# Optimization experiments

Hardware: AMD Instinct MI355X
Metric: run time of the kernel (lower is better)

## Reference

```python
import jax, jax.numpy as jnp
import numpy as np

N_NODES = 100000
N_EDGES = 1600000
IN_C, HID_C, OUT_C = 128, 128, 64


def setup_inputs() -> dict:
    key = jax.random.key(0)
    k1, k2, k3, k4 = jax.random.split(key, 4)
    x = jax.random.normal(k1, (N_NODES, IN_C), dtype=jnp.float32)
    edge_index = jax.random.randint(k2, (2, N_EDGES), 0, N_NODES, dtype=jnp.int32)
    # Glorot-style init scale for the linear weights (matches PyG GCNConv default)
    W1 = jax.random.normal(k3, (IN_C, HID_C), dtype=jnp.float32) * (1.0 / np.sqrt(IN_C))
    b1 = jnp.zeros((HID_C,), dtype=jnp.float32)
    W2 = jax.random.normal(k4, (HID_C, OUT_C), dtype=jnp.float32) * (1.0 / np.sqrt(HID_C))
    b2 = jnp.zeros((OUT_C,), dtype=jnp.float32)
    return {"x": x, "edge_index": edge_index, "W1": W1, "b1": b1, "W2": W2, "b2": b2}


def _gcn_norm(edge_index, num_nodes):
    """Add self-loops and compute symmetric normalization deg^-1/2[src]*deg^-1/2[dst]."""
    src, dst = edge_index[0], edge_index[1]
    loop = jnp.arange(num_nodes, dtype=src.dtype)
    src_f = jnp.concatenate([src, loop])
    dst_f = jnp.concatenate([dst, loop])
    ones = jnp.ones_like(dst_f, dtype=jnp.float32)
    deg = jax.ops.segment_sum(ones, dst_f, num_segments=num_nodes)  # in-degree incl. self-loop
    deg_inv_sqrt = jnp.where(deg > 0, jax.lax.rsqrt(deg), 0.0)
    norm = deg_inv_sqrt[src_f] * deg_inv_sqrt[dst_f]  # [E+N]
    return src_f, dst_f, norm


def _gcn_conv(x, W, b, src_f, dst_f, norm, num_nodes):
    h = x @ W                              # [N, C_out] linear transform first
    msg = h[src_f] * norm[:, None]         # gather + scale, [E+N, C_out]
    agg = jax.ops.segment_sum(msg, dst_f, num_segments=num_nodes)  # scatter-add
    return agg + b


def reference(x, edge_index, W1, b1, W2, b2):
    n = x.shape[0]
    src_f, dst_f, norm = _gcn_norm(edge_index, n)
    h = jax.nn.relu(_gcn_conv(x, W1, b1, src_f, dst_f, norm, n))
    out = _gcn_conv(h, W2, b2, src_f, dst_f, norm, n)
    return out
```

## Files before the change

kernel.cpp:

```cpp
#include <hip/hip_runtime.h>


constexpr int BLK = 256;
constexpr int PCAP = 2560;
constexpr int CHUNK = 2048;
constexpr int NBMAX = 800;


__global__ __launch_bounds__(256)
void count_kernel(const int* __restrict__ dst, unsigned short* __restrict__ cnt,
                  int e, int nbuck) {
    __shared__ int hist[NBMAX];
    const int t = threadIdx.x;
    const int base = blockIdx.x * CHUNK;
    const int cend = min(CHUNK, e - base);

    for (int i = t; i < nbuck; i += 256) hist[i] = 0;
    __syncthreads();
    for (int i = t; i < cend; i += 256) atomicAdd(&hist[dst[base + i] >> 7], 1);
    __syncthreads();
    unsigned short* o = cnt + (size_t)blockIdx.x * nbuck;
    for (int i = t; i < nbuck; i += 256) o[i] = (unsigned short)hist[i];
}


__global__ __launch_bounds__(256)
void scan_bins_kernel(unsigned short* __restrict__ cnt, int* __restrict__ totals,
                      int nbuck, int nblk) {
    __shared__ int wsum[256];
    const int j = blockIdx.x;
    const int t = threadIdx.x;
    const int b0 = t * 4;
    int v[4];
    int s = 0;
#pragma unroll
    for (int q = 0; q < 4; ++q) {
        const int B = b0 + q;
        v[q] = (B < nblk) ? (int)cnt[(size_t)B * nbuck + j] : 0;
        s += v[q];
    }
    wsum[t] = s;
    __syncthreads();
    for (int off = 1; off < 256; off <<= 1) {
        int u = (t >= off) ? wsum[t - off] : 0;
        __syncthreads();
        wsum[t] += u;
        __syncthreads();
    }
    int run = (t > 0) ? wsum[t - 1] : 0;
#pragma unroll
    for (int q = 0; q < 4; ++q) {
        const int B = b0 + q;
        if (B < nblk) {
            cnt[(size_t)B * nbuck + j] = (unsigned short)min(run, PCAP);
            run += v[q];
        }
    }
    if (t == 255) totals[j] = run;
}


__global__ __launch_bounds__(256)
void place_kernel(const int* __restrict__ src, const int* __restrict__ dst,
                  const unsigned short* __restrict__ cnt, unsigned* __restrict__ ebuf,
                  int e, int nbuck) {
    __shared__ unsigned stage[CHUNK];
    __shared__ unsigned short keys[CHUNK];
    __shared__ int hist[NBMAX];
    __shared__ int excl[NBMAX];
    __shared__ int gbase[NBMAX];
    __shared__ int wsum[256];

    const int t = threadIdx.x;
    const int base = blockIdx.x * CHUNK;
    const int cend = min(CHUNK, e - base);

    for (int i = t; i < nbuck; i += 256) hist[i] = 0;
    __syncthreads();

    int dreg[8];
#pragma unroll
    for (int q = 0; q < 8; ++q) {
        const int i = t + q * 256;
        dreg[q] = (i < cend) ? dst[base + i] : -1;
        if (i < cend) atomicAdd(&hist[dreg[q] >> 7], 1);
    }
    __syncthreads();

    const int b0 = t * 4;
    int s0 = 0, s1 = 0, s2 = 0, s3 = 0;
    if (b0 < nbuck)     s0 = hist[b0];
    if (b0 + 1 < nbuck) s1 = hist[b0 + 1];
    if (b0 + 2 < nbuck) s2 = hist[b0 + 2];
    if (b0 + 3 < nbuck) s3 = hist[b0 + 3];
    wsum[t] = s0 + s1 + s2 + s3;
    __syncthreads();
    for (int off = 1; off < 256; off <<= 1) {
        int u = (t >= off) ? wsum[t - off] : 0;
        __syncthreads();
        wsum[t] += u;
        __syncthreads();
    }
    int run = (t > 0) ? wsum[t - 1] : 0;
    if (b0 < nbuck)     { excl[b0]     = run; hist[b0]     = run; run += s0; }
    if (b0 + 1 < nbuck) { excl[b0 + 1] = run; hist[b0 + 1] = run; run += s1; }
    if (b0 + 2 < nbuck) { excl[b0 + 2] = run; hist[b0 + 2] = run; run += s2; }
    if (b0 + 3 < nbuck) { excl[b0 + 3] = run; hist[b0 + 3] = run; run += s3; }
    {
        const unsigned short* cb = cnt + (size_t)blockIdx.x * nbuck;
        for (int i = t; i < nbuck; i += 256) gbase[i] = (int)cb[i];
    }
    __syncthreads();

#pragma unroll
    for (int q = 0; q < 8; ++q) {
        const int i = t + q * 256;
        if (i < cend) {
            const int s = src[base + i], d = dreg[q];
            const int bb = d >> 7;
            const int p = atomicAdd(&hist[bb], 1);
            stage[p] = ((unsigned)s << 7) | (unsigned)(d & 127);
            keys[p] = (unsigned short)bb;
        }
    }
    __syncthreads();

    for (int i = t; i < cend; i += 256) {
        const int bb = keys[i];
        const int p = gbase[bb] + (i - excl[bb]);
        if (p < PCAP) ebuf[(size_t)bb * PCAP + p] = stage[i];
    }
}


__global__ __launch_bounds__(256)
void build_kernel(const unsigned* __restrict__ ebuf, const int* __restrict__ totals,
                  float* __restrict__ dis, int2* __restrict__ rp,
                  int* __restrict__ esrc, int n) {
    __shared__ int packed[PCAP];
    __shared__ int sorted[PCAP];
    __shared__ unsigned short rank[PCAP];
    __shared__ int hist[128];
    __shared__ int excl[128];
    __shared__ int start[128];

    const int b = blockIdx.x, t = threadIdx.x;
    const int base = b << 7;
    const int nloc = min(128, n - base);
    const int tot = min(totals[b], PCAP);

    if (t < 128) hist[t] = 0;
    __syncthreads();

    const unsigned* eb = ebuf + (size_t)b * PCAP;
    for (int i = t; i < tot; i += 256) {
        int v = (int)eb[i];
        packed[i] = v;
        rank[i] = (unsigned short)atomicAdd(&hist[v & 127], 1);
    }
    __syncthreads();

    if (t < 128) excl[t] = hist[t];
    __syncthreads();
    for (int off = 1; off < 128; off <<= 1) {
        int v = (t >= off && t < 128) ? excl[t - off] : 0;
        __syncthreads();
        if (t < 128) excl[t] += v;
        __syncthreads();
    }

    if (t < 128) {
        int deg = hist[t];
        int st = excl[t] - deg;
        start[t] = st;
        if (t < nloc) {
            dis[base + t] = rsqrtf((float)(deg + 1));
            int gs = b * PCAP + st;
            rp[base + t] = make_int2(gs, gs + deg);
        }
    }
    __syncthreads();

    for (int i = t; i < tot; i += 256) {
        int v = packed[i];
        sorted[start[v & 127] + rank[i]] = v >> 7;
    }
    __syncthreads();

    if (t < 128) {
        const int s0 = start[t];
        const int e0 = s0 + hist[t];
        for (int i = s0 + 1; i < e0; ++i) {
            int v = sorted[i];
            int j = i - 1;
            while (j >= s0 && sorted[j] > v) { sorted[j + 1] = sorted[j]; --j; }
            sorted[j + 1] = v;
        }
    }
    __syncthreads();

    int* eo = esrc + b * PCAP;
    for (int i = t; i < tot; i += 256) eo[i] = sorted[i];
}


__device__ __forceinline__ unsigned short f2bf(float f) {
    unsigned u = __float_as_uint(f);
    u += 0x7fffu + ((u >> 16) & 1u);
    return (unsigned short)(u >> 16);
}
__device__ __forceinline__ float bflo(unsigned u) { return __uint_as_float(u << 16); }
__device__ __forceinline__ float bfhi(unsigned u) { return __uint_as_float(u & 0xffff0000u); }
__device__ __forceinline__ unsigned pk2(short a, short b) {
    return (unsigned)(unsigned short)a | ((unsigned)(unsigned short)b << 16);
}

__device__ __forceinline__ void split2(float v, short& hi, short& lo) {
    unsigned short h = f2bf(v);
    float hf = __uint_as_float(((unsigned)h) << 16);
    hi = (short)h;
    lo = (short)f2bf(v - hf);
}

typedef __attribute__((ext_vector_type(8))) short bf16x8;
typedef __attribute__((ext_vector_type(4))) float f32x4;
#define MFMA_B16(a, b, c) __builtin_amdgcn_mfma_f32_16x16x32_bf16(a, b, c, 0, 0, 0)

__device__ __forceinline__ void split8(const float4& a, const float4& b, bf16x8& h, bf16x8& l) {
    short hh, ll;
    split2(a.x, hh, ll); h[0] = hh; l[0] = ll;
    split2(a.y, hh, ll); h[1] = hh; l[1] = ll;
    split2(a.z, hh, ll); h[2] = hh; l[2] = ll;
    split2(a.w, hh, ll); h[3] = hh; l[3] = ll;
    split2(b.x, hh, ll); h[4] = hh; l[4] = ll;
    split2(b.y, hh, ll); h[5] = hh; l[5] = ll;
    split2(b.z, hh, ll); h[6] = hh; l[6] = ll;
    split2(b.w, hh, ll); h[7] = hh; l[7] = ll;
}


__global__ void prep_b_kernel(const float* __restrict__ W1, const float* __restrict__ W2,
                              unsigned short* __restrict__ B1h, unsigned short* __restrict__ B1l,
                              unsigned short* __restrict__ B2h, unsigned short* __restrict__ B2l) {
    const int c = blockIdx.x;
    const int k = threadIdx.x;
    short h, l;
    if (c < 128) {
        split2(W1[(size_t)k * 128 + c], h, l);
        B1h[c * 128 + k] = (unsigned short)h;
        B1l[c * 128 + k] = (unsigned short)l;
    } else {
        const int c2 = c - 128;
        split2(W2[(size_t)k * 64 + c2], h, l);
        B2h[c2 * 128 + k] = (unsigned short)h;
        B2l[c2 * 128 + k] = (unsigned short)l;
    }
}


constexpr int BAS = 72;

__global__ __launch_bounds__(256, 4)
void gemm_mfma(const float* __restrict__ Af,
               const unsigned short* __restrict__ Bh, const unsigned short* __restrict__ Bl,
               const float* __restrict__ dis, unsigned* __restrict__ Cb, int nrows) {
    constexpr int COLS = 128;
    constexpr int CT = COLS / 16;
    constexpr int BE = COLS * BAS;
    constexpr int CSC = COLS + 8;
    constexpr int SMEM = (2 * BE * 2 > 128 * CSC * 2) ? 2 * BE * 2 : 128 * CSC * 2;

    __shared__ __align__(16) char smem[SMEM];
    short* sBh = (short*)smem;
    short* sBl = sBh + BE;

    const int t = threadIdx.x;
    const int rowbase = blockIdx.x * 128;
    const int wave = t >> 6;
    const int lane = t & 63;
    const int quad = lane >> 4;
    const int l16 = lane & 15;

    const int gr0 = rowbase + wave * 32 + l16;
    const int gr1 = gr0 + 16;

    f32x4 acc[2][CT];
#pragma unroll
    for (int rt = 0; rt < 2; ++rt)
#pragma unroll
        for (int ct = 0; ct < CT; ++ct) {
            f32x4 z = {0.f, 0.f, 0.f, 0.f};
            acc[rt][ct] = z;
        }

    for (int half = 0; half < 2; ++half) {
        {
            constexpr int NV = COLS * 8;
            uint4* dh = (uint4*)sBh;
            uint4* dl = (uint4*)sBl;
            const uint4* gh = (const uint4*)Bh;
            const uint4* gl = (const uint4*)Bl;
            for (int idx = t; idx < NV; idx += 256) {
                int c = idx >> 3, kq = idx & 7;
                int gidx = c * 16 + half * 8 + kq;
                int didx = c * 9 + kq;
                dh[didx] = gh[gidx];
                dl[didx] = gl[gidx];
            }
        }
        __syncthreads();

#pragma unroll
        for (int kc = 0; kc < 2; ++kc) {
            const int ko = kc * 32 + quad * 8;
            bf16x8 ah0, al0, ah1, al1;
            float4 va = {0.f, 0.f, 0.f, 0.f}, vb = va, vc = va, vd = va;
            if (gr0 < nrows) {
                const float4* ap = (const float4*)(Af + (size_t)gr0 * 128 + half * 64 + ko);
                va = ap[0]; vb = ap[1];
            }
            if (gr1 < nrows) {
                const float4* ap = (const float4*)(Af + (size_t)gr1 * 128 + half * 64 + ko);
                vc = ap[0]; vd = ap[1];
            }
            split8(va, vb, ah0, al0);
            split8(vc, vd, ah1, al1);
#pragma unroll
            for (int ct = 0; ct < CT; ++ct) {
                const int bo = (ct * 16 + l16) * BAS + ko;
                bf16x8 bh = *(const bf16x8*)&sBh[bo];
                bf16x8 bl = *(const bf16x8*)&sBl[bo];
                acc[0][ct] = MFMA_B16(ah0, bh, acc[0][ct]);
                acc[1][ct] = MFMA_B16(ah1, bh, acc[1][ct]);
                acc[0][ct] = MFMA_B16(al0, bh, acc[0][ct]);
                acc[1][ct] = MFMA_B16(al1, bh, acc[1][ct]);
                acc[0][ct] = MFMA_B16(ah0, bl, acc[0][ct]);
                acc[1][ct] = MFMA_B16(ah1, bl, acc[1][ct]);
            }
        }
        __syncthreads();
    }

    short* Cs = (short*)smem;
    float sv[2][4];
#pragma unroll
    for (int rt = 0; rt < 2; ++rt)
#pragma unroll
        for (int r = 0; r < 4; ++r) {
            int rr = rowbase + wave * 32 + rt * 16 + quad * 4 + r;
            sv[rt][r] = (rr < nrows) ? dis[rr] : 0.f;
        }
#pragma unroll
    for (int rt = 0; rt < 2; ++rt)
#pragma unroll
        for (int ct = 0; ct < CT; ++ct) {
            const int rb = wave * 32 + rt * 16 + quad * 4;
            const int c = ct * 16 + l16;
#pragma unroll
            for (int r = 0; r < 4; ++r)
                Cs[(rb + r) * CSC + c] = (short)f2bf(sv[rt][r] * acc[rt][ct][r]);
        }
    __syncthreads();

    {
        const int row = t >> 1, hf = t & 1;
        const int gr = rowbase + row;
        if (gr < nrows) {
            const uint4* cr = (const uint4*)&Cs[row * CSC + hf * (COLS / 2)];
            uint4* dstp = (uint4*)Cb + (size_t)gr * (COLS / 8) + hf * (COLS / 16);
#pragma unroll
            for (int i = 0; i < COLS / 16; ++i) dstp[i] = cr[i];
        }
    }
}


#define ACC8(v)                                           \
    acc[0] += bflo(v.x); acc[1] += bfhi(v.x);             \
    acc[2] += bflo(v.y); acc[3] += bfhi(v.y);             \
    acc[4] += bflo(v.z); acc[5] += bfhi(v.z);             \
    acc[6] += bflo(v.w); acc[7] += bfhi(v.w);

__global__ __launch_bounds__(512)
void gather_gemm_kernel(const int2* __restrict__ rp, const int* __restrict__ esrc,
                        const float* __restrict__ dis, const unsigned* __restrict__ hs,
                        const float* __restrict__ bias,
                        const unsigned short* __restrict__ B2h,
                        const unsigned short* __restrict__ B2l,
                        unsigned* __restrict__ h2b, int n) {
    constexpr int ASTR = 136;
    constexpr int CSTR = 72;
    __shared__ __align__(16) short sAh[32 * ASTR];
    __shared__ __align__(16) short sAl[32 * ASTR];

    const int t = threadIdx.x;
    const int base = blockIdx.x * 32;

    {
        const int nl = t >> 4;
        const int lc = t & 15;
        const int node = base + nl;

        if (node < n) {
            const uint4* h4 = (const uint4*)hs;
            const int2 se = rp[node];
            float acc[8];
            {
                uint4 v = h4[(size_t)node * 16 + lc];
                acc[0] = bflo(v.x); acc[1] = bfhi(v.x);
                acc[2] = bflo(v.y); acc[3] = bfhi(v.y);
                acc[4] = bflo(v.z); acc[5] = bfhi(v.z);
                acc[6] = bflo(v.w); acc[7] = bfhi(v.w);
            }
            int k = se.x;
            const int end = se.y;
            for (; k + 3 < end; k += 4) {
                int s0 = esrc[k], s1 = esrc[k + 1], s2 = esrc[k + 2], s3 = esrc[k + 3];
                uint4 v0 = h4[(size_t)s0 * 16 + lc];
                uint4 v1 = h4[(size_t)s1 * 16 + lc];
                uint4 v2 = h4[(size_t)s2 * 16 + lc];
                uint4 v3 = h4[(size_t)s3 * 16 + lc];
                ACC8(v0) ACC8(v1) ACC8(v2) ACC8(v3)
            }
            for (; k < end; ++k) {
                uint4 v = h4[(size_t)esrc[k] * 16 + lc];
                ACC8(v)
            }

            const float di = dis[node];
            const float4 ba = ((const float4*)bias)[lc * 2];
            const float4 bb = ((const float4*)bias)[lc * 2 + 1];
            float v0 = fmaxf(fmaf(di, acc[0], ba.x), 0.f);
            float v1 = fmaxf(fmaf(di, acc[1], ba.y), 0.f);
            float v2 = fmaxf(fmaf(di, acc[2], ba.z), 0.f);
            float v3 = fmaxf(fmaf(di, acc[3], ba.w), 0.f);
            float v4 = fmaxf(fmaf(di, acc[4], bb.x), 0.f);
            float v5 = fmaxf(fmaf(di, acc[5], bb.y), 0.f);
            float v6 = fmaxf(fmaf(di, acc[6], bb.z), 0.f);
            float v7 = fmaxf(fmaf(di, acc[7], bb.w), 0.f);

            short h0, l0, h1, l1, h2, l2, h3, l3, h4v, l4, h5, l5, h6, l6, h7, l7;
            split2(v0, h0, l0); split2(v1, h1, l1); split2(v2, h2, l2); split2(v3, h3, l3);
            split2(v4, h4v, l4); split2(v5, h5, l5); split2(v6, h6, l6); split2(v7, h7, l7);
            uint4 oh, ol;
            oh.x = pk2(h0, h1); oh.y = pk2(h2, h3); oh.z = pk2(h4v, h5); oh.w = pk2(h6, h7);
            ol.x = pk2(l0, l1); ol.y = pk2(l2, l3); ol.z = pk2(l4, l5);  ol.w = pk2(l6, l7);
            *(uint4*)&sAh[nl * ASTR + lc * 8] = oh;
            *(uint4*)&sAl[nl * ASTR + lc * 8] = ol;
        } else {
            uint4 z = {0u, 0u, 0u, 0u};
            *(uint4*)&sAh[nl * ASTR + lc * 8] = z;
            *(uint4*)&sAl[nl * ASTR + lc * 8] = z;
        }
    }
    __syncthreads();

    const int wave = t >> 6, lane = t & 63, quad = lane >> 4, l16 = lane & 15;
    const int col = wave * 16 + l16;
    f32x4 c0 = {0.f, 0.f, 0.f, 0.f}, c1 = c0;
    if (t < 256) {
#pragma unroll
        for (int ks = 0; ks < 4; ++ks) {
            const int ko = ks * 32 + quad * 8;
            bf16x8 bh = *(const bf16x8*)&B2h[col * 128 + ko];
            bf16x8 bl = *(const bf16x8*)&B2l[col * 128 + ko];
            bf16x8 ah0 = *(const bf16x8*)&sAh[l16 * ASTR + ko];
            bf16x8 al0 = *(const bf16x8*)&sAl[l16 * ASTR + ko];
            bf16x8 ah1 = *(const bf16x8*)&sAh[(16 + l16) * ASTR + ko];
            bf16x8 al1 = *(const bf16x8*)&sAl[(16 + l16) * ASTR + ko];
            c0 = MFMA_B16(ah0, bh, c0);
            c1 = MFMA_B16(ah1, bh, c1);
            c0 = MFMA_B16(al0, bh, c0);
            c1 = MFMA_B16(al1, bh, c1);
            c0 = MFMA_B16(ah0, bl, c0);
            c1 = MFMA_B16(ah1, bl, c1);
        }
    }
    __syncthreads();

    short* Cs = sAh;
    if (t < 256) {
#pragma unroll
        for (int r = 0; r < 4; ++r) {
            const int row0 = quad * 4 + r, row1 = 16 + quad * 4 + r;
            const float d0 = (base + row0 < n) ? dis[base + row0] : 0.f;
            const float d1 = (base + row1 < n) ? dis[base + row1] : 0.f;
            Cs[row0 * CSTR + col] = (short)f2bf(d0 * c0[r]);
            Cs[row1 * CSTR + col] = (short)f2bf(d1 * c1[r]);
        }
    }
    __syncthreads();
    if (t < 256) {
        const int row = t >> 3, l8 = t & 7;
        const int gr = base + row;
        if (gr < n)
            ((uint4*)h2b)[(size_t)gr * 8 + l8] = *(const uint4*)&Cs[row * CSTR + l8 * 8];
    }
}


#define ACCLO(v)                                          \
    acc[0] += bflo(v.x); acc[1] += bfhi(v.x);             \
    acc[2] += bflo(v.y); acc[3] += bfhi(v.y);             \
    acc[4] += bflo(v.z); acc[5] += bfhi(v.z);             \
    acc[6] += bflo(v.w); acc[7] += bfhi(v.w);
#define ACCHI(v)                                          \
    acc[8]  += bflo(v.x); acc[9]  += bfhi(v.x);           \
    acc[10] += bflo(v.y); acc[11] += bfhi(v.y);           \
    acc[12] += bflo(v.z); acc[13] += bfhi(v.z);           \
    acc[14] += bflo(v.w); acc[15] += bfhi(v.w);

__global__ __launch_bounds__(256)
void gather_out_kernel(const int2* __restrict__ rp, const int* __restrict__ esrc,
                       const float* __restrict__ dis, const unsigned* __restrict__ hs,
                       const float* __restrict__ bias, float* __restrict__ out, int n) {
    const int gid = blockIdx.x * BLK + threadIdx.x;
    const int node = gid >> 2;
    const int l4 = gid & 3;
    if (node >= n) return;

    const uint4* h4 = (const uint4*)hs;
    const int2 se = rp[node];

    float acc[16];
    {
        uint4 v0 = h4[(size_t)node * 8 + l4];
        uint4 v1 = h4[(size_t)node * 8 + 4 + l4];
        acc[0] = bflo(v0.x); acc[1] = bfhi(v0.x);
        acc[2] = bflo(v0.y); acc[3] = bfhi(v0.y);
        acc[4] = bflo(v0.z); acc[5] = bfhi(v0.z);
        acc[6] = bflo(v0.w); acc[7] = bfhi(v0.w);
        acc[8]  = bflo(v1.x); acc[9]  = bfhi(v1.x);
        acc[10] = bflo(v1.y); acc[11] = bfhi(v1.y);
        acc[12] = bflo(v1.z); acc[13] = bfhi(v1.z);
        acc[14] = bflo(v1.w); acc[15] = bfhi(v1.w);
    }

    int k = se.x;
    const int end = se.y;
    for (; k + 3 < end; k += 4) {
        int s0 = esrc[k], s1 = esrc[k + 1], s2 = esrc[k + 2], s3 = esrc[k + 3];
        uint4 a0 = h4[(size_t)s0 * 8 + l4], b0 = h4[(size_t)s0 * 8 + 4 + l4];
        uint4 a1 = h4[(size_t)s1 * 8 + l4], b1 = h4[(size_t)s1 * 8 + 4 + l4];
        uint4 a2 = h4[(size_t)s2 * 8 + l4], b2 = h4[(size_t)s2 * 8 + 4 + l4];
        uint4 a3 = h4[(size_t)s3 * 8 + l4], b3 = h4[(size_t)s3 * 8 + 4 + l4];
        ACCLO(a0) ACCHI(b0) ACCLO(a1) ACCHI(b1)
        ACCLO(a2) ACCHI(b2) ACCLO(a3) ACCHI(b3)
    }
    for (; k < end; ++k) {
        int s = esrc[k];
        uint4 a = h4[(size_t)s * 8 + l4], b = h4[(size_t)s * 8 + 4 + l4];
        ACCLO(a) ACCHI(b)
    }

    const float di = dis[node];
    const float4* b4 = (const float4*)bias;
    const float4 ba = b4[l4 * 2], bb = b4[l4 * 2 + 1];
    const float4 bc = b4[8 + l4 * 2], bd = b4[9 + l4 * 2];
    float4 o0, o1, o2, o3;
    o0.x = fmaf(di, acc[0],  ba.x); o0.y = fmaf(di, acc[1],  ba.y);
    o0.z = fmaf(di, acc[2],  ba.z); o0.w = fmaf(di, acc[3],  ba.w);
    o1.x = fmaf(di, acc[4],  bb.x); o1.y = fmaf(di, acc[5],  bb.y);
    o1.z = fmaf(di, acc[6],  bb.z); o1.w = fmaf(di, acc[7],  bb.w);
    o2.x = fmaf(di, acc[8],  bc.x); o2.y = fmaf(di, acc[9],  bc.y);
    o2.z = fmaf(di, acc[10], bc.z); o2.w = fmaf(di, acc[11], bc.w);
    o3.x = fmaf(di, acc[12], bd.x); o3.y = fmaf(di, acc[13], bd.y);
    o3.z = fmaf(di, acc[14], bd.z); o3.w = fmaf(di, acc[15], bd.w);
    float4* o4 = (float4*)out;
    o4[(size_t)node * 16 + l4 * 2]     = o0;
    o4[(size_t)node * 16 + l4 * 2 + 1] = o1;
    o4[(size_t)node * 16 + 8 + l4 * 2]     = o2;
    o4[(size_t)node * 16 + 8 + l4 * 2 + 1] = o3;
}

#undef ACC8
#undef ACCLO
#undef ACCHI


extern "C" void kernel_launch(void* const* d_in, const int* in_sizes, int n_in,
                              void* d_out, int out_size, void* d_ws, size_t ws_size,
                              hipStream_t stream) {
    const float* x  = (const float*)d_in[0];
    const int*   ei = (const int*)d_in[1];
    const float* W1 = (const float*)d_in[2];
    const float* b1 = (const float*)d_in[3];
    const float* W2 = (const float*)d_in[4];
    const float* b2 = (const float*)d_in[5];
    float* out = (float*)d_out;

    const int n = in_sizes[0] / 128;
    const int e = in_sizes[1] / 2;
    const int* src = ei;
    const int* dst = ei + e;

    char* ws = (char*)d_ws;
    float*    dis    = (float*)   (ws + 0x0);
    int2*     rp     = (int2*)    (ws + 0x80000);
    int*      totals = (int*)     (ws + 0x180000);
    unsigned short* B1h = (unsigned short*)(ws + 0x182000);
    unsigned short* B1l = (unsigned short*)(ws + 0x18A000);
    unsigned short* B2h = (unsigned short*)(ws + 0x192000);
    unsigned short* B2l = (unsigned short*)(ws + 0x196000);
    unsigned short* cnt = (unsigned short*)(ws + 0x1A0000);
    int*      esrc = (int*)     (ws + 0x2E0000);
    unsigned* hb   = (unsigned*)(ws + 0xB00000);
    unsigned* h2b  = (unsigned*)(ws + 0x2400000);
    unsigned* ebuf = (unsigned*)(ws + 0x2400000);

    const int nbuck = (n + 127) >> 7;
    const int nblk = (e + CHUNK - 1) / CHUNK;
    const int nb_g = (n + 127) / 128;

    prep_b_kernel<<<192, 128, 0, stream>>>(W1, W2, B1h, B1l, B2h, B2l);
    count_kernel<<<nblk, 256, 0, stream>>>(dst, cnt, e, nbuck);
    scan_bins_kernel<<<nbuck, 256, 0, stream>>>(cnt, totals, nbuck, nblk);
    place_kernel<<<nblk, 256, 0, stream>>>(src, dst, cnt, ebuf, e, nbuck);
    build_kernel<<<nbuck, 256, 0, stream>>>(ebuf, totals, dis, rp, esrc, n);

    gemm_mfma<<<nb_g, 256, 0, stream>>>(x, B1h, B1l, dis, hb, n);

    gather_gemm_kernel<<<(n + 31) / 32, 512, 0, stream>>>(
        rp, esrc, dis, hb, b1, B2h, B2l, h2b, n);

    gather_out_kernel<<<(n * 4 + BLK - 1) / BLK, BLK, 0, stream>>>(
        rp, esrc, dis, h2b, b2, out, n);
}
```

Measured before the change: 305.1 us.

## Slice second-layer features by channel group and drop per-node source sorting

The second-layer hidden features are now stored as four channel slices of 16 bf16 values each, one contiguous array per slice. The output gather kernel gives each thread a whole node within one slice, with blocks interleaved across slices. Each slice's working set becomes smaller and more cache-friendly, and consecutive threads read from many nodes instead of four threads sharing a row. The build kernel also skips the per-node insertion sort of source indices and writes unsorted neighbours directly to global memory, removing shared-memory sorting work at the cost of less ordered gather access.

Result: no change. 305.7 us (+0.2%).

```diff
diff --git a/kernel.cpp b/kernel.cpp
--- a/kernel.cpp
+++ b/kernel.cpp
@@ -138,7 +138,6 @@
                   float* __restrict__ dis, int2* __restrict__ rp,
                   int* __restrict__ esrc, int n) {
     __shared__ int packed[PCAP];
-    __shared__ int sorted[PCAP];
     __shared__ unsigned short rank[PCAP];
     __shared__ int hist[128];
     __shared__ int excl[128];
@@ -181,26 +180,11 @@
     }
     __syncthreads();
 
+    int* eo = esrc + b * PCAP;
     for (int i = t; i < tot; i += 256) {
         int v = packed[i];
-        sorted[start[v & 127] + rank[i]] = v >> 7;
-    }
-    __syncthreads();
-
-    if (t < 128) {
-        const int s0 = start[t];
-        const int e0 = s0 + hist[t];
-        for (int i = s0 + 1; i < e0; ++i) {
-            int v = sorted[i];
-            int j = i - 1;
-            while (j >= s0 && sorted[j] > v) { sorted[j + 1] = sorted[j]; --j; }
-            sorted[j + 1] = v;
-        }
-    }
-    __syncthreads();
-
-    int* eo = esrc + b * PCAP;
-    for (int i = t; i < tot; i += 256) eo[i] = sorted[i];
+        eo[start[v & 127] + rank[i]] = v >> 7;
+    }
 }
 
 
@@ -493,8 +477,11 @@
     if (t < 256) {
         const int row = t >> 3, l8 = t & 7;
         const int gr = base + row;
-        if (gr < n)
-            ((uint4*)h2b)[(size_t)gr * 8 + l8] = *(const uint4*)&Cs[row * CSTR + l8 * 8];
+        if (gr < n) {
+            const int sl = l8 >> 1, w = l8 & 1;
+            ((uint4*)h2b)[((size_t)sl * n + gr) * 2 + w] =
+                *(const uint4*)&Cs[row * CSTR + l8 * 8];
+        }
     }
 }
 
@@ -511,21 +498,21 @@
     acc[14] += bflo(v.w); acc[15] += bfhi(v.w);
 
 __global__ __launch_bounds__(256)
-void gather_out_kernel(const int2* __restrict__ rp, const int* __restrict__ esrc,
-                       const float* __restrict__ dis, const unsigned* __restrict__ hs,
-                       const float* __restrict__ bias, float* __restrict__ out, int n) {
-    const int gid = blockIdx.x * BLK + threadIdx.x;
-    const int node = gid >> 2;
-    const int l4 = gid & 3;
+void gather_out_slice_kernel(const int2* __restrict__ rp, const int* __restrict__ esrc,
+                             const float* __restrict__ dis, const unsigned* __restrict__ hs,
+                             const float* __restrict__ bias, float* __restrict__ out, int n) {
+    const int slice = blockIdx.x & 3;
+    const int tile = blockIdx.x >> 2;
+    const int node = tile * 256 + threadIdx.x;
     if (node >= n) return;
 
-    const uint4* h4 = (const uint4*)hs;
+    const uint4* h4 = (const uint4*)hs + (size_t)slice * n * 2;
     const int2 se = rp[node];
 
     float acc[16];
     {
-        uint4 v0 = h4[(size_t)node * 8 + l4];
-        uint4 v1 = h4[(size_t)node * 8 + 4 + l4];
+        uint4 v0 = h4[(size_t)node * 2];
+        uint4 v1 = h4[(size_t)node * 2 + 1];
         acc[0] = bflo(v0.x); acc[1] = bfhi(v0.x);
         acc[2] = bflo(v0.y); acc[3] = bfhi(v0.y);
         acc[4] = bflo(v0.z); acc[5] = bfhi(v0.z);
@@ -540,23 +527,22 @@
     const int end = se.y;
     for (; k + 3 < end; k += 4) {
         int s0 = esrc[k], s1 = esrc[k + 1], s2 = esrc[k + 2], s3 = esrc[k + 3];
-        uint4 a0 = h4[(size_t)s0 * 8 + l4], b0 = h4[(size_t)s0 * 8 + 4 + l4];
-        uint4 a1 = h4[(size_t)s1 * 8 + l4], b1 = h4[(size_t)s1 * 8 + 4 + l4];
-        uint4 a2 = h4[(size_t)s2 * 8 + l4], b2 = h4[(size_t)s2 * 8 + 4 + l4];
-        uint4 a3 = h4[(size_t)s3 * 8 + l4], b3 = h4[(size_t)s3 * 8 + 4 + l4];
+        uint4 a0 = h4[(size_t)s0 * 2], b0 = h4[(size_t)s0 * 2 + 1];
+        uint4 a1 = h4[(size_t)s1 * 2], b1 = h4[(size_t)s1 * 2 + 1];
+        uint4 a2 = h4[(size_t)s2 * 2], b2 = h4[(size_t)s2 * 2 + 1];
+        uint4 a3 = h4[(size_t)s3 * 2], b3 = h4[(size_t)s3 * 2 + 1];
         ACCLO(a0) ACCHI(b0) ACCLO(a1) ACCHI(b1)
         ACCLO(a2) ACCHI(b2) ACCLO(a3) ACCHI(b3)
     }
     for (; k < end; ++k) {
         int s = esrc[k];
-        uint4 a = h4[(size_t)s * 8 + l4], b = h4[(size_t)s * 8 + 4 + l4];
+        uint4 a = h4[(size_t)s * 2], b = h4[(size_t)s * 2 + 1];
         ACCLO(a) ACCHI(b)
     }
 
     const float di = dis[node];
-    const float4* b4 = (const float4*)bias;
-    const float4 ba = b4[l4 * 2], bb = b4[l4 * 2 + 1];
-    const float4 bc = b4[8 + l4 * 2], bd = b4[9 + l4 * 2];
+    const float4* b4 = (const float4*)bias + slice * 4;
+    const float4 ba = b4[0], bb = b4[1], bc = b4[2], bd = b4[3];
     float4 o0, o1, o2, o3;
     o0.x = fmaf(di, acc[0],  ba.x); o0.y = fmaf(di, acc[1],  ba.y);
     o0.z = fmaf(di, acc[2],  ba.z); o0.w = fmaf(di, acc[3],  ba.w);
@@ -566,11 +552,8 @@
     o2.z = fmaf(di, acc[10], bc.z); o2.w = fmaf(di, acc[11], bc.w);
     o3.x = fmaf(di, acc[12], bd.x); o3.y = fmaf(di, acc[13], bd.y);
     o3.z = fmaf(di, acc[14], bd.z); o3.w = fmaf(di, acc[15], bd.w);
-    float4* o4 = (float4*)out;
-    o4[(size_t)node * 16 + l4 * 2]     = o0;
-    o4[(size_t)node * 16 + l4 * 2 + 1] = o1;
-    o4[(size_t)node * 16 + 8 + l4 * 2]     = o2;
-    o4[(size_t)node * 16 + 8 + l4 * 2 + 1] = o3;
+    float4* o4 = (float4*)out + (size_t)node * 16 + slice * 4;
+    o4[0] = o0; o4[1] = o1; o4[2] = o2; o4[3] = o3;
 }
 
 #undef ACC8
@@ -623,6 +606,6 @@
     gather_gemm_kernel<<<(n + 31) / 32, 512, 0, stream>>>(
         rp, esrc, dis, hb, b1, B2h, B2l, h2b, n);
 
-    gather_out_kernel<<<(n * 4 + BLK - 1) / BLK, BLK, 0, stream>>>(
+    gather_out_slice_kernel<<<((n + 255) / 256) * 4, 256, 0, stream>>>(
         rp, esrc, dis, h2b, b2, out, n);
 }
```
